# Kernel optimization log

Hardware: AMD Instinct MI355X
Metric: run time of the kernel (lower is better)

The kernel has to match this reference:

```python
import jax, jax.numpy as jnp
import numpy as np

E = 1024
H = 16
CH = E // H

def setup_inputs() -> dict:
    key = jax.random.key(0)
    ks = jax.random.split(key, 9)
    s = E ** -0.5
    return {
        'x': jax.random.normal(ks[0], (4, 2048, E), dtype=jnp.float32),
        'Wq': jax.random.normal(ks[1], (E, E), dtype=jnp.float32) * s,
        'bq': jnp.zeros((E,), dtype=jnp.float32),
        'Wk': jax.random.normal(ks[2], (E, E), dtype=jnp.float32) * s,
        'bk': jnp.zeros((E,), dtype=jnp.float32),
        'Wv': jax.random.normal(ks[3], (E, E), dtype=jnp.float32) * s,
        'bv': jnp.zeros((E,), dtype=jnp.float32),
        'Wo': jax.random.normal(ks[4], (E, E), dtype=jnp.float32) * s,
        'bo': jnp.zeros((E,), dtype=jnp.float32),
    }

def _split_heads(t):
    # [..., n, H*ch] -> [..., H, n, ch]
    b, n, e = t.shape
    return t.reshape(b, n, H, CH).transpose(0, 2, 1, 3)

def reference(x, Wq, bq, Wk, bk, Wv, bv, Wo, bo):
    scale = CH ** -0.5
    q = _split_heads(x @ Wq.T + bq)  # [b,H,n,ch]
    k = _split_heads(x @ Wk.T + bk)
    v = _split_heads(x @ Wv.T + bv)
    att = jnp.einsum('bhqc,bhkc->bhqk', q, k) * scale
    att = jax.nn.softmax(att, axis=-1)
    out = jnp.einsum('bhqk,bhkc->bhqc', att, v)  # [b,H,n,ch]
    b, h, n, c = out.shape
    out = out.transpose(0, 2, 1, 3).reshape(b, n, h * c)
    return out @ Wo.T + bo
```

## Files before the change

### kernel.cpp

```cpp
#include <hip/hip_runtime.h>
#include <stdint.h>

#define EMB   1024
#define NHEAD 16
#define CHD   64
#define NB    4
#define SEQ   2048
#define NTOK  (NB * SEQ)
#define KDIM  1024

typedef __attribute__((ext_vector_type(8))) short  bf16x8;
typedef __attribute__((ext_vector_type(4))) short  short4v;
typedef __attribute__((ext_vector_type(4))) float  f32x4;
typedef __attribute__((ext_vector_type(4))) float  float4v;

__device__ __forceinline__ short f2bf(float f) {
    unsigned int u = __float_as_uint(f);
    u += 0x7fffu + ((u >> 16) & 1u);
    return (short)(u >> 16);
}

__device__ __forceinline__ void async16(const short* g, short* l) {
    __builtin_amdgcn_global_load_lds((__attribute__((address_space(1))) void const*)g,
                                     (__attribute__((address_space(3))) void*)l, 16, 0, 0);
}

__global__ __launch_bounds__(256) void cvt_bf16(const float* __restrict__ in,
                                                short* __restrict__ out, int n4) {
    int i = blockIdx.x * 256 + threadIdx.x;
    if (i < n4) {
        float4v v = ((const float4v*)in)[i];
        short4v s;
        s.x = f2bf(v.x); s.y = f2bf(v.y); s.z = f2bf(v.z); s.w = f2bf(v.w);
        ((short4v*)out)[i] = s;
    }
}

__device__ __forceinline__ void gemm_core(const short* __restrict__ Atile,
                                          const short* __restrict__ Btile,
                                          short* As, short* Bs, f32x4 acc[4][4]) {
    const int tid  = threadIdx.x;
    const int wave = tid >> 6, lane = tid & 63;
    const int quad = lane >> 4, l16 = lane & 15;
    const int wm = (wave >> 1) * 64, wn = (wave & 1) * 64;
    const int srow = lane >> 2;
    const int scol = (lane & 3) * 8;

    for (int k0 = 0; k0 < KDIM; k0 += 32) {
        __syncthreads();
#pragma unroll
        for (int c = 0; c < 2; ++c) {
            int chunk = wave * 2 + c;
            int row = chunk * 16 + srow;
            async16(Atile + (size_t)row * KDIM + k0 + scol, As + chunk * 512);
            async16(Btile + (size_t)row * KDIM + k0 + scol, Bs + chunk * 512);
        }
        __syncthreads();
        bf16x8 af[4], bfr[4];
#pragma unroll
        for (int i = 0; i < 4; ++i)
            af[i] = *(const bf16x8*)&As[(wm + i * 16 + l16) * 32 + quad * 8];
#pragma unroll
        for (int j = 0; j < 4; ++j)
            bfr[j] = *(const bf16x8*)&Bs[(wn + j * 16 + l16) * 32 + quad * 8];
#pragma unroll
        for (int i = 0; i < 4; ++i)
#pragma unroll
            for (int j = 0; j < 4; ++j)
                acc[i][j] = __builtin_amdgcn_mfma_f32_16x16x32_bf16(af[i], bfr[j], acc[i][j], 0, 0, 0);
    }
}

__global__ __launch_bounds__(256) void qkv_gemm(const short* __restrict__ xb,
                                                const short* __restrict__ Wqb,
                                                const short* __restrict__ Wkb,
                                                const short* __restrict__ Wvb,
                                                const float* __restrict__ bq,
                                                const float* __restrict__ bk,
                                                const float* __restrict__ bv,
                                                short* __restrict__ Qb,
                                                short* __restrict__ Kb,
                                                short* __restrict__ Vtb) {
    __shared__ short As[128 * 32], Bs[128 * 32];
    const int bm = blockIdx.x, bn = blockIdx.y;
    const int which = bn >> 3;
    const int ew = (bn & 7) * 128;
    const short* W    = (which == 0) ? Wqb : (which == 1) ? Wkb : Wvb;
    const float* bias = (which == 0) ? bq  : (which == 1) ? bk  : bv;
    const float sc    = (which == 0) ? 0.125f : 1.0f;

    f32x4 acc[4][4];
    const f32x4 z = {0.f, 0.f, 0.f, 0.f};
#pragma unroll
    for (int i = 0; i < 4; ++i)
#pragma unroll
        for (int j = 0; j < 4; ++j) acc[i][j] = z;

    gemm_core(xb + (size_t)bm * 128 * KDIM, W + (size_t)ew * KDIM, As, Bs, acc);

    const int lane = threadIdx.x & 63, wave = threadIdx.x >> 6;
    const int quad = lane >> 4, l16 = lane & 15;
    const int wm = (wave >> 1) * 64, wn = (wave & 1) * 64;
#pragma unroll
    for (int i = 0; i < 4; ++i)
#pragma unroll
        for (int j = 0; j < 4; ++j)
#pragma unroll
            for (int r = 0; r < 4; ++r) {
                int row_l = wm + i * 16 + quad * 4 + r;
                int col_l = wn + j * 16 + l16;
                int token = bm * 128 + row_l;
                int bb = token >> 11, nn = token & 2047;
                int e = ew + col_l;
                short h = f2bf((acc[i][j][r] + bias[e]) * sc);
                int hh = e >> 6, cc = e & 63;
                if (which == 2)
                    Vtb[(((size_t)bb * NHEAD + hh) * CHD + cc) * SEQ + nn] = h;
                else {
                    short* dst = which ? Kb : Qb;
                    dst[(((size_t)bb * NHEAD + hh) * SEQ + nn) * CHD + cc] = h;
                }
            }
}

__global__ __launch_bounds__(256, 4) void attn(const short* __restrict__ Qb,
                                               const short* __restrict__ Kb,
                                               const short* __restrict__ Vtb,
                                               short* __restrict__ AOb) {
    __shared__ short Ks[16 * 512];
    __shared__ short Vs[16 * 512];

    const int qt = blockIdx.x;
    const int bh = blockIdx.y;
    const int tid = threadIdx.x, wave = tid >> 6, lane = tid & 63;
    const int quad = lane >> 4, l16 = lane & 15;

    const short* Kg = Kb  + (size_t)bh * SEQ * CHD;
    const short* Vg = Vtb + (size_t)bh * CHD * SEQ;

    const short* Qg = Qb + ((size_t)bh * SEQ + qt * 64 + wave * 16 + l16) * CHD;
    bf16x8 qf0 = *(const bf16x8*)(Qg + quad * 8);
    bf16x8 qf1 = *(const bf16x8*)(Qg + 32 + quad * 8);

    const int kr = lane >> 3, ku = (lane & 7) ^ kr;
    const int vr = lane >> 4, vu = (lane & 15) ^ (vr << 2);

    const int krow = l16 & 7;
    const int kbase = ((l16 >> 3) * 512) + krow * 64;
    const int vrow = l16 & 3;
    const int vbase0 = (l16 >> 2) * 512 + vrow * 128;

    f32x4 O[4];
    const f32x4 z = {0.f, 0.f, 0.f, 0.f};
#pragma unroll
    for (int nb = 0; nb < 4; ++nb) O[nb] = z;
    float lsum = 0.f;

    for (int kt = 0; kt < 16; ++kt) {
        __syncthreads();
#pragma unroll
        for (int cc = 0; cc < 4; ++cc) {
            int c = wave * 4 + cc;
            int l = c * 8 + kr;
            int j = l >> 4, m = l & 15;
            int kvg = ((j >> 1) << 5) + ((m >> 2) << 3) + ((j & 1) << 2) + (m & 3);
            async16(Kg + ((size_t)(kt * 128 + kvg)) * CHD + ku * 8, Ks + c * 512);
            async16(Vg + (size_t)(c * 4 + vr) * SEQ + kt * 128 + vu * 8, Vs + c * 512);
        }
        __syncthreads();

        f32x4 sacc[8];
#pragma unroll
        for (int j = 0; j < 8; ++j) sacc[j] = z;
#pragma unroll
        for (int j = 0; j < 8; ++j) {
            int b0 = j * 1024 + kbase + ((quad ^ krow) << 3);
            int b1 = j * 1024 + kbase + (((4 + quad) ^ krow) << 3);
            bf16x8 k0 = *(const bf16x8*)&Ks[b0];
            bf16x8 k1 = *(const bf16x8*)&Ks[b1];
            sacc[j] = __builtin_amdgcn_mfma_f32_16x16x32_bf16(k0, qf0, sacc[j], 0, 0, 0);
            sacc[j] = __builtin_amdgcn_mfma_f32_16x16x32_bf16(k1, qf1, sacc[j], 0, 0, 0);
        }

#pragma unroll
        for (int kk = 0; kk < 4; ++kk) {
            int d[4];
#pragma unroll
            for (int t = 0; t < 2; ++t) {
                f32x4 s4 = sacc[2 * kk + t];
                unsigned u0 = __float_as_uint(__expf(s4.x));
                unsigned u1 = __float_as_uint(__expf(s4.y));
                unsigned u2 = __float_as_uint(__expf(s4.z));
                unsigned u3 = __float_as_uint(__expf(s4.w));
                lsum += __uint_as_float(u0 & 0xffff0000u) + __uint_as_float(u1 & 0xffff0000u)
                      + __uint_as_float(u2 & 0xffff0000u) + __uint_as_float(u3 & 0xffff0000u);
                d[2 * t]     = __builtin_amdgcn_perm(u1, u0, 0x07060302u);
                d[2 * t + 1] = __builtin_amdgcn_perm(u3, u2, 0x07060302u);
            }
            union { int i[4]; bf16x8 v; } pf;
            pf.i[0] = d[0]; pf.i[1] = d[1]; pf.i[2] = d[2]; pf.i[3] = d[3];
#pragma unroll
            for (int nb = 0; nb < 4; ++nb) {
                int vb = nb * 2048 + vbase0 + ((((kk << 2) + quad) ^ (vrow << 2)) << 3);
                bf16x8 vf = *(const bf16x8*)&Vs[vb];
                O[nb] = __builtin_amdgcn_mfma_f32_16x16x32_bf16(pf.v, vf, O[nb], 0, 0, 0);
            }
        }
    }

    lsum += __shfl_xor(lsum, 16);
    lsum += __shfl_xor(lsum, 32);
    float linv[4];
#pragma unroll
    for (int r = 0; r < 4; ++r)
        linv[r] = 1.0f / __shfl(lsum, quad * 4 + r);

    const int b = bh >> 4, h = bh & 15;
#pragma unroll
    for (int nb = 0; nb < 4; ++nb)
#pragma unroll
        for (int r = 0; r < 4; ++r) {
            int n = qt * 64 + wave * 16 + quad * 4 + r;
            int cc = nb * 16 + l16;
            AOb[((size_t)b * SEQ + n) * EMB + h * CHD + cc] = f2bf(O[nb][r] * linv[r]);
        }
}

__global__ __launch_bounds__(256) void out_gemm(const short* __restrict__ AOb,
                                                const short* __restrict__ Wob,
                                                const float* __restrict__ bo,
                                                float* __restrict__ out) {
    __shared__ short As[128 * 32], Bs[128 * 32];
    const int bm = blockIdx.x, bn = blockIdx.y;

    f32x4 acc[4][4];
    const f32x4 z = {0.f, 0.f, 0.f, 0.f};
#pragma unroll
    for (int i = 0; i < 4; ++i)
#pragma unroll
        for (int j = 0; j < 4; ++j) acc[i][j] = z;

    gemm_core(AOb + (size_t)bm * 128 * KDIM, Wob + (size_t)bn * 128 * KDIM, As, Bs, acc);

    const int lane = threadIdx.x & 63, wave = threadIdx.x >> 6;
    const int quad = lane >> 4, l16 = lane & 15;
    const int wm = (wave >> 1) * 64, wn = (wave & 1) * 64;
#pragma unroll
    for (int i = 0; i < 4; ++i)
#pragma unroll
        for (int j = 0; j < 4; ++j)
#pragma unroll
            for (int r = 0; r < 4; ++r) {
                int token = bm * 128 + wm + i * 16 + quad * 4 + r;
                int e = bn * 128 + wn + j * 16 + l16;
                out[(size_t)token * EMB + e] = acc[i][j][r] + bo[e];
            }
}

extern "C" void kernel_launch(void* const* d_in, const int* in_sizes, int n_in,
                              void* d_out, int out_size, void* d_ws, size_t ws_size,
                              hipStream_t stream) {
    const float* x  = (const float*)d_in[0];
    const float* Wq = (const float*)d_in[1];
    const float* bq = (const float*)d_in[2];
    const float* Wk = (const float*)d_in[3];
    const float* bk = (const float*)d_in[4];
    const float* Wv = (const float*)d_in[5];
    const float* bv = (const float*)d_in[6];
    const float* Wo = (const float*)d_in[7];
    const float* bo = (const float*)d_in[8];

    char* ws = (char*)d_ws;
    short* xb  = (short*)(ws + 0);
    short* Wqb = (short*)(ws + (size_t)16 * 1024 * 1024);
    short* Wkb = (short*)(ws + (size_t)18 * 1024 * 1024);
    short* Wvb = (short*)(ws + (size_t)20 * 1024 * 1024);
    short* Wob = (short*)(ws + (size_t)22 * 1024 * 1024);
    short* Qb  = (short*)(ws + (size_t)24 * 1024 * 1024);
    short* Kb  = (short*)(ws + (size_t)40 * 1024 * 1024);
    short* Vtb = (short*)(ws + (size_t)56 * 1024 * 1024);
    short* AOb = (short*)(ws + (size_t)72 * 1024 * 1024);

    cvt_bf16<<<dim3(8192), dim3(256), 0, stream>>>(x, xb, NTOK * EMB / 4);
    cvt_bf16<<<dim3(1024), dim3(256), 0, stream>>>(Wq, Wqb, EMB * EMB / 4);
    cvt_bf16<<<dim3(1024), dim3(256), 0, stream>>>(Wk, Wkb, EMB * EMB / 4);
    cvt_bf16<<<dim3(1024), dim3(256), 0, stream>>>(Wv, Wvb, EMB * EMB / 4);
    cvt_bf16<<<dim3(1024), dim3(256), 0, stream>>>(Wo, Wob, EMB * EMB / 4);

    qkv_gemm<<<dim3(64, 24), dim3(256), 0, stream>>>(xb, Wqb, Wkb, Wvb, bq, bk, bv, Qb, Kb, Vtb);
    attn<<<dim3(32, 64), dim3(256), 0, stream>>>(Qb, Kb, Vtb, AOb);
    out_gemm<<<dim3(64, 8), dim3(256), 0, stream>>>(AOb, Wob, bo, (float*)d_out);
}
```

Before: 312.5 us.

## Fuse conversions, transpose V GEMM, use exp2 and MFMA row sums in attention

Merges the five fp32-to-bf16 conversion launches into one kernel. The V projection now computes W·xᵀ, so the stores into the transposed V buffer become contiguous along the sequence. Attention folds log2(e) into the Q scale and calls the hardware exp2, replaces the scalar row-sum plus shuffles with an MFMA against a ones vector, and precomputes the async-load and LDS addresses outside the key loop. Each tile adds one extra MFMA, and the row sum is now built from bf16-rounded probabilities.

New measurement: 287.5 us. -8.0%, faster.

```diff
diff --git a/kernel.cpp b/kernel.cpp
--- a/kernel.cpp
+++ b/kernel.cpp
@@ -25,15 +25,33 @@
                                      (__attribute__((address_space(3))) void*)l, 16, 0, 0);
 }
 
-__global__ __launch_bounds__(256) void cvt_bf16(const float* __restrict__ in,
-                                                short* __restrict__ out, int n4) {
-    int i = blockIdx.x * 256 + threadIdx.x;
-    if (i < n4) {
-        float4v v = ((const float4v*)in)[i];
-        short4v s;
-        s.x = f2bf(v.x); s.y = f2bf(v.y); s.z = f2bf(v.z); s.w = f2bf(v.w);
-        ((short4v*)out)[i] = s;
-    }
+__global__ __launch_bounds__(256) void cvt_all(const float* __restrict__ x,
+                                               const float* __restrict__ Wq,
+                                               const float* __restrict__ Wk,
+                                               const float* __restrict__ Wv,
+                                               const float* __restrict__ Wo,
+                                               short* __restrict__ xb,
+                                               short* __restrict__ Wqb,
+                                               short* __restrict__ Wkb,
+                                               short* __restrict__ Wvb,
+                                               short* __restrict__ Wob) {
+    int bid = blockIdx.x;
+    const float* src;
+    short* dst;
+    int idx;
+    if (bid < 8192) {
+        src = x; dst = xb; idx = bid * 256 + threadIdx.x;
+    } else {
+        int w  = (bid - 8192) >> 10;
+        int lb = (bid - 8192) & 1023;
+        src = (w == 0) ? Wq : (w == 1) ? Wk : (w == 2) ? Wv : Wo;
+        dst = (w == 0) ? Wqb : (w == 1) ? Wkb : (w == 2) ? Wvb : Wob;
+        idx = lb * 256 + threadIdx.x;
+    }
+    float4v v = ((const float4v*)src)[idx];
+    short4v s;
+    s.x = f2bf(v.x); s.y = f2bf(v.y); s.z = f2bf(v.z); s.w = f2bf(v.w);
+    ((short4v*)dst)[idx] = s;
 }
 
 __device__ __forceinline__ void gemm_core(const short* __restrict__ Atile,
@@ -71,6 +89,7 @@
     }
 }
 
+#define QSCALE 0.1803368801111204f
 __global__ __launch_bounds__(256) void qkv_gemm(const short* __restrict__ xb,
                                                 const short* __restrict__ Wqb,
                                                 const short* __restrict__ Wkb,
@@ -87,7 +106,12 @@
     const int ew = (bn & 7) * 128;
     const short* W    = (which == 0) ? Wqb : (which == 1) ? Wkb : Wvb;
     const float* bias = (which == 0) ? bq  : (which == 1) ? bk  : bv;
-    const float sc    = (which == 0) ? 0.125f : 1.0f;
+    const float sc    = (which == 0) ? QSCALE : 1.0f;
+
+    const short* Xt = xb + (size_t)bm * 128 * KDIM;
+    const short* Wt = W + (size_t)ew * KDIM;
+    const short* Ap = (which == 2) ? Wt : Xt;
+    const short* Bp = (which == 2) ? Xt : Wt;
 
     f32x4 acc[4][4];
     const f32x4 z = {0.f, 0.f, 0.f, 0.f};
@@ -96,31 +120,42 @@
 #pragma unroll
         for (int j = 0; j < 4; ++j) acc[i][j] = z;
 
-    gemm_core(xb + (size_t)bm * 128 * KDIM, W + (size_t)ew * KDIM, As, Bs, acc);
+    gemm_core(Ap, Bp, As, Bs, acc);
 
     const int lane = threadIdx.x & 63, wave = threadIdx.x >> 6;
     const int quad = lane >> 4, l16 = lane & 15;
     const int wm = (wave >> 1) * 64, wn = (wave & 1) * 64;
-#pragma unroll
-    for (int i = 0; i < 4; ++i)
-#pragma unroll
-        for (int j = 0; j < 4; ++j)
-#pragma unroll
-            for (int r = 0; r < 4; ++r) {
-                int row_l = wm + i * 16 + quad * 4 + r;
-                int col_l = wn + j * 16 + l16;
-                int token = bm * 128 + row_l;
-                int bb = token >> 11, nn = token & 2047;
-                int e = ew + col_l;
-                short h = f2bf((acc[i][j][r] + bias[e]) * sc);
-                int hh = e >> 6, cc = e & 63;
-                if (which == 2)
-                    Vtb[(((size_t)bb * NHEAD + hh) * CHD + cc) * SEQ + nn] = h;
-                else {
-                    short* dst = which ? Kb : Qb;
-                    dst[(((size_t)bb * NHEAD + hh) * SEQ + nn) * CHD + cc] = h;
+
+    if (which == 2) {
+#pragma unroll
+        for (int i = 0; i < 4; ++i)
+#pragma unroll
+            for (int j = 0; j < 4; ++j)
+#pragma unroll
+                for (int r = 0; r < 4; ++r) {
+                    int e = ew + wm + i * 16 + quad * 4 + r;
+                    int token = bm * 128 + wn + j * 16 + l16;
+                    int bb = token >> 11, nn = token & 2047;
+                    int hh = e >> 6, cc = e & 63;
+                    Vtb[(((size_t)bb * NHEAD + hh) * CHD + cc) * SEQ + nn] =
+                        f2bf(acc[i][j][r] + bias[e]);
                 }
-            }
+    } else {
+        short* dst = which ? Kb : Qb;
+#pragma unroll
+        for (int i = 0; i < 4; ++i)
+#pragma unroll
+            for (int j = 0; j < 4; ++j)
+#pragma unroll
+                for (int r = 0; r < 4; ++r) {
+                    int token = bm * 128 + wm + i * 16 + quad * 4 + r;
+                    int bb = token >> 11, nn = token & 2047;
+                    int e = ew + wn + j * 16 + l16;
+                    int hh = e >> 6, cc = e & 63;
+                    dst[(((size_t)bb * NHEAD + hh) * SEQ + nn) * CHD + cc] =
+                        f2bf((acc[i][j][r] + bias[e]) * sc);
+                }
+    }
 }
 
 __global__ __launch_bounds__(256, 4) void attn(const short* __restrict__ Qb,
@@ -145,41 +180,53 @@
     const int kr = lane >> 3, ku = (lane & 7) ^ kr;
     const int vr = lane >> 4, vu = (lane & 15) ^ (vr << 2);
 
+    int koff[4], voff[4];
+#pragma unroll
+    for (int cc = 0; cc < 4; ++cc) {
+        int c = wave * 4 + cc;
+        int l = c * 8 + kr;
+        int j = l >> 4, m = l & 15;
+        int kvg = ((j >> 1) << 5) + ((m >> 2) << 3) + ((j & 1) << 2) + (m & 3);
+        koff[cc] = kvg * CHD + ku * 8;
+        voff[cc] = (c * 4 + vr) * SEQ + vu * 8;
+    }
+
     const int krow = l16 & 7;
     const int kbase = ((l16 >> 3) * 512) + krow * 64;
+    const short* kp0 = Ks + kbase + ((quad ^ krow) << 3);
+    const short* kp1 = Ks + kbase + (((4 + quad) ^ krow) << 3);
     const int vrow = l16 & 3;
-    const int vbase0 = (l16 >> 2) * 512 + vrow * 128;
-
+    const short* vp = Vs + (l16 >> 2) * 512 + vrow * 128 + quad * 8;
+
+    const f32x4 zf = {0.f, 0.f, 0.f, 0.f};
+    const bf16x8 onesv = {16256, 16256, 16256, 16256, 16256, 16256, 16256, 16256};
     f32x4 O[4];
-    const f32x4 z = {0.f, 0.f, 0.f, 0.f};
-#pragma unroll
-    for (int nb = 0; nb < 4; ++nb) O[nb] = z;
-    float lsum = 0.f;
+#pragma unroll
+    for (int nb = 0; nb < 4; ++nb) O[nb] = zf;
+    f32x4 lacc = zf;
+
+    const short* Kgp = Kg;
+    const short* Vgp = Vg;
 
     for (int kt = 0; kt < 16; ++kt) {
         __syncthreads();
 #pragma unroll
         for (int cc = 0; cc < 4; ++cc) {
             int c = wave * 4 + cc;
-            int l = c * 8 + kr;
-            int j = l >> 4, m = l & 15;
-            int kvg = ((j >> 1) << 5) + ((m >> 2) << 3) + ((j & 1) << 2) + (m & 3);
-            async16(Kg + ((size_t)(kt * 128 + kvg)) * CHD + ku * 8, Ks + c * 512);
-            async16(Vg + (size_t)(c * 4 + vr) * SEQ + kt * 128 + vu * 8, Vs + c * 512);
-        }
+            async16(Kgp + koff[cc], Ks + c * 512);
+            async16(Vgp + voff[cc], Vs + c * 512);
+        }
+        Kgp += 128 * CHD;
+        Vgp += 128;
         __syncthreads();
 
         f32x4 sacc[8];
 #pragma unroll
-        for (int j = 0; j < 8; ++j) sacc[j] = z;
-#pragma unroll
         for (int j = 0; j < 8; ++j) {
-            int b0 = j * 1024 + kbase + ((quad ^ krow) << 3);
-            int b1 = j * 1024 + kbase + (((4 + quad) ^ krow) << 3);
-            bf16x8 k0 = *(const bf16x8*)&Ks[b0];
-            bf16x8 k1 = *(const bf16x8*)&Ks[b1];
-            sacc[j] = __builtin_amdgcn_mfma_f32_16x16x32_bf16(k0, qf0, sacc[j], 0, 0, 0);
-            sacc[j] = __builtin_amdgcn_mfma_f32_16x16x32_bf16(k1, qf1, sacc[j], 0, 0, 0);
+            bf16x8 k0 = *(const bf16x8*)(kp0 + j * 1024);
+            bf16x8 k1 = *(const bf16x8*)(kp1 + j * 1024);
+            f32x4 t = __builtin_amdgcn_mfma_f32_16x16x32_bf16(k0, qf0, zf, 0, 0, 0);
+            sacc[j] = __builtin_amdgcn_mfma_f32_16x16x32_bf16(k1, qf1, t, 0, 0, 0);
         }
 
 #pragma unroll
@@ -188,32 +235,28 @@
 #pragma unroll
             for (int t = 0; t < 2; ++t) {
                 f32x4 s4 = sacc[2 * kk + t];
-                unsigned u0 = __float_as_uint(__expf(s4.x));
-                unsigned u1 = __float_as_uint(__expf(s4.y));
-                unsigned u2 = __float_as_uint(__expf(s4.z));
-                unsigned u3 = __float_as_uint(__expf(s4.w));
-                lsum += __uint_as_float(u0 & 0xffff0000u) + __uint_as_float(u1 & 0xffff0000u)
-                      + __uint_as_float(u2 & 0xffff0000u) + __uint_as_float(u3 & 0xffff0000u);
+                unsigned u0 = __float_as_uint(__builtin_amdgcn_exp2f(s4.x));
+                unsigned u1 = __float_as_uint(__builtin_amdgcn_exp2f(s4.y));
+                unsigned u2 = __float_as_uint(__builtin_amdgcn_exp2f(s4.z));
+                unsigned u3 = __float_as_uint(__builtin_amdgcn_exp2f(s4.w));
                 d[2 * t]     = __builtin_amdgcn_perm(u1, u0, 0x07060302u);
                 d[2 * t + 1] = __builtin_amdgcn_perm(u3, u2, 0x07060302u);
             }
             union { int i[4]; bf16x8 v; } pf;
             pf.i[0] = d[0]; pf.i[1] = d[1]; pf.i[2] = d[2]; pf.i[3] = d[3];
+            lacc = __builtin_amdgcn_mfma_f32_16x16x32_bf16(pf.v, onesv, lacc, 0, 0, 0);
+            const short* vpk = vp + ((kk ^ vrow) << 5);
 #pragma unroll
             for (int nb = 0; nb < 4; ++nb) {
-                int vb = nb * 2048 + vbase0 + ((((kk << 2) + quad) ^ (vrow << 2)) << 3);
-                bf16x8 vf = *(const bf16x8*)&Vs[vb];
+                bf16x8 vf = *(const bf16x8*)(vpk + nb * 2048);
                 O[nb] = __builtin_amdgcn_mfma_f32_16x16x32_bf16(pf.v, vf, O[nb], 0, 0, 0);
             }
         }
     }
 
-    lsum += __shfl_xor(lsum, 16);
-    lsum += __shfl_xor(lsum, 32);
     float linv[4];
 #pragma unroll
-    for (int r = 0; r < 4; ++r)
-        linv[r] = 1.0f / __shfl(lsum, quad * 4 + r);
+    for (int r = 0; r < 4; ++r) linv[r] = 1.0f / lacc[r];
 
     const int b = bh >> 4, h = bh & 15;
 #pragma unroll
@@ -281,12 +324,8 @@
     short* Vtb = (short*)(ws + (size_t)56 * 1024 * 1024);
     short* AOb = (short*)(ws + (size_t)72 * 1024 * 1024);
 
-    cvt_bf16<<<dim3(8192), dim3(256), 0, stream>>>(x, xb, NTOK * EMB / 4);
-    cvt_bf16<<<dim3(1024), dim3(256), 0, stream>>>(Wq, Wqb, EMB * EMB / 4);
-    cvt_bf16<<<dim3(1024), dim3(256), 0, stream>>>(Wk, Wkb, EMB * EMB / 4);
-    cvt_bf16<<<dim3(1024), dim3(256), 0, stream>>>(Wv, Wvb, EMB * EMB / 4);
-    cvt_bf16<<<dim3(1024), dim3(256), 0, stream>>>(Wo, Wob, EMB * EMB / 4);
-
+    cvt_all<<<dim3(8192 + 4096), dim3(256), 0, stream>>>(x, Wq, Wk, Wv, Wo,
+                                                         xb, Wqb, Wkb, Wvb, Wob);
     qkv_gemm<<<dim3(64, 24), dim3(256), 0, stream>>>(xb, Wqb, Wkb, Wvb, bq, bk, bv, Qb, Kb, Vtb);
     attn<<<dim3(32, 64), dim3(256), 0, stream>>>(Qb, Kb, Vtb, AOb);
     out_gemm<<<dim3(64, 8), dim3(256), 0, stream>>>(AOb, Wob, bo, (float*)d_out);
```
